# Kernel tuning notes

Hardware: AMD Instinct MI355X
Metric: run time of the kernel (lower is better)

Reference implementation:

```python
import jax, jax.numpy as jnp
import numpy as np

B, N_E, E_DIM = 131072, 1024, 64
BETA = 0.25


def setup_inputs() -> dict:
    key = jax.random.key(0)
    kz, kw = jax.random.split(key)
    z = jax.random.normal(kz, (B, E_DIM), dtype=jnp.float32)
    # nn.Embedding init: uniform(-1/n_e, 1/n_e)
    emb_w = jax.random.uniform(kw, (N_E, E_DIM), dtype=jnp.float32,
                               minval=-1.0 / N_E, maxval=1.0 / N_E)
    return {"z": z, "emb_w": emb_w}


def reference(z, emb_w):
    beta = jnp.float32(BETA)
    # pairwise squared distances: [B, n_e]
    d = (jnp.sum(z * z, axis=1, keepdims=True)
         + jnp.sum(emb_w * emb_w, axis=1)
         - 2.0 * jnp.einsum('bd,nd->bn', z, emb_w))
    idx = jnp.argmin(d, axis=1)                      # [B]
    z_q = jnp.take(emb_w, idx, axis=0)               # [B, e_dim]
    # legacy=False branch
    loss = (beta * jnp.mean((jax.lax.stop_gradient(z_q) - z) ** 2)
            + jnp.mean((z_q - jax.lax.stop_gradient(z)) ** 2))
    # straight-through estimator
    z_q_st = z + jax.lax.stop_gradient(z_q - z)
    # torch.var is unbiased (ddof=1)
    v = jnp.var(idx.astype(jnp.float32), ddof=1)
    return (z_q_st, loss, idx, v)
```

## Files before the change

kernel.cpp:

```cpp
#include <hip/hip_runtime.h>
#include <stdint.h>


typedef __attribute__((ext_vector_type(8))) __bf16 bf16x8;
typedef __attribute__((ext_vector_type(4))) float f32x4;

#define OUT_LOSS 8388608
#define OUT_IDX  8388609
#define OUT_VAR  8519681

#define WS_LOSS  0
#define WS_S1    4096
#define WS_S2    8192
#define WS_EFRAG 12288
#define WS_EE    143360

__device__ __forceinline__ void gld_lds16(const void* g, void* l) {
  __builtin_amdgcn_global_load_lds(
      (const __attribute__((address_space(1))) unsigned*)g,
      (__attribute__((address_space(3))) unsigned*)l, 16, 0, 0);
}

__global__ void vq_prep(const float* __restrict__ emb, char* __restrict__ ws) {
  bf16x8* efrag = (bf16x8*)(ws + WS_EFRAG);
  float* eeoff = (float*)(ws + WS_EE);
  const int t = blockIdx.x;
  const int l = threadIdx.x;
  const int n = t * 16 + (l & 15);
  const int kb0 = (l >> 4) * 8;
  const float* er = emb + n * 64;
  for (int j = 0; j < 2; ++j) {
    const int kb = j * 32 + kb0;
    bf16x8 h;
#pragma unroll
    for (int i = 0; i < 8; ++i) h[i] = (__bf16)(-2.0f * er[kb + i]);
    efrag[(t * 2 + j) * 64 + l] = h;
  }
  if (l < 16) {
    const float* e2 = emb + (t * 16 + l) * 64;
    float s = 0.f;
#pragma unroll
    for (int d = 0; d < 64; ++d) s += e2[d] * e2[d];
    eeoff[t * 16 + l] = s + 0.5f;
  }
}

__global__ void __launch_bounds__(256) vq_main(
    const float* __restrict__ z, const float* __restrict__ emb,
    float* __restrict__ out, char* __restrict__ ws) {
  __shared__ char smfrag[3][16384];
  __shared__ float see[1024];
  __shared__ float sL[4];
  __shared__ int sA[4], sB[4];

  const int tid = threadIdx.x;
  const int wave = tid >> 6, lane = tid & 63;
  const int lr = lane & 15, ksl = lane >> 4;
  const int k0 = ksl * 8;
  const int row_base = blockIdx.x * 256 + wave * 64;

#define STAGE(ph, buf)                                                          \
  {                                                                             \
    _Pragma("unroll")                                                           \
    for (int i_ = 0; i_ < 4; ++i_)                                              \
      gld_lds16(ws + WS_EFRAG + (ph) * 16384 + wave * 4096 + i_ * 1024 + lane * 16, \
                smfrag[buf] + wave * 4096 + i_ * 1024);                         \
  }

  f32x4 zr[16];
#pragma unroll
  for (int r = 0; r < 4; ++r) {
    const float* zp = z + (size_t)(row_base + r * 16 + lr) * 64;
    zr[r * 4 + 0] = *(const f32x4*)(zp + k0);
    zr[r * 4 + 1] = *(const f32x4*)(zp + k0 + 4);
    zr[r * 4 + 2] = *(const f32x4*)(zp + 32 + k0);
    zr[r * 4 + 3] = *(const f32x4*)(zp + 32 + k0 + 4);
  }

  gld_lds16(ws + WS_EE + wave * 1024 + lane * 16, (char*)see + wave * 1024);
  STAGE(0, 0);
  STAGE(1, 1);

  bf16x8 zf[4][2];
  float zz[4];
#pragma unroll
  for (int r = 0; r < 4; ++r) {
    float s = 0.f;
#pragma unroll
    for (int i = 0; i < 4; ++i) {
      zf[r][0][i] = (__bf16)zr[r * 4 + 0][i]; zf[r][0][4 + i] = (__bf16)zr[r * 4 + 1][i];
      zf[r][1][i] = (__bf16)zr[r * 4 + 2][i]; zf[r][1][4 + i] = (__bf16)zr[r * 4 + 3][i];
      s += zr[r * 4 + 0][i] * zr[r * 4 + 0][i] + zr[r * 4 + 1][i] * zr[r * 4 + 1][i]
         + zr[r * 4 + 2][i] * zr[r * 4 + 2][i] + zr[r * 4 + 3][i] * zr[r * 4 + 3][i];
    }
    s += __shfl_xor(s, 16, 64);
    s += __shfl_xor(s, 32, 64);
    zz[r] = s;
  }

  unsigned rk[4];
#pragma unroll
  for (int r = 0; r < 4; ++r) rk[r] = 0xFFFFFFFFu;
  const unsigned kj0 = (unsigned)(ksl * 4), kj1 = kj0 + 1, kj2 = kj0 + 2, kj3 = kj0 + 3;

  for (int ph = 0; ph < 8; ++ph) {
    if (ph < 7) { asm volatile("s_waitcnt vmcnt(4)" ::: "memory"); }
    else        { asm volatile("s_waitcnt vmcnt(0)" ::: "memory"); }
    __builtin_amdgcn_sched_barrier(0);
    __builtin_amdgcn_s_barrier();
    if (ph < 6) STAGE(ph + 2, (ph + 2) % 3);
    const bf16x8* sfrag = (const bf16x8*)(smfrag[ph % 3]);
    __builtin_amdgcn_s_setprio(1);
#pragma unroll
    for (int half = 0; half < 2; ++half) {
      bf16x8 E0[4], E1[4];
      f32x4 EE[4];
#pragma unroll
      for (int q = 0; q < 4; ++q) {
        const int tt = half * 4 + q;
        E0[q] = sfrag[(tt * 2 + 0) * 64 + lane];
        E1[q] = sfrag[(tt * 2 + 1) * 64 + lane];
        EE[q] = *(const f32x4*)(see + (ph * 8 + tt) * 16 + ksl * 4);
      }
#pragma unroll
      for (int q = 0; q < 4; ++q) {
        const unsigned g16 = (unsigned)((ph * 8 + half * 4 + q) * 16);
#pragma unroll
        for (int r = 0; r < 4; ++r) {
          f32x4 a = __builtin_amdgcn_mfma_f32_16x16x32_bf16(E0[q], zf[r][0], EE[q], 0, 0, 0);
          a = __builtin_amdgcn_mfma_f32_16x16x32_bf16(E1[q], zf[r][1], a, 0, 0, 0);
          const unsigned t0 = (__float_as_uint(a[0]) & 0xFFFFFC00u) | kj0;
          const unsigned t1 = (__float_as_uint(a[1]) & 0xFFFFFC00u) | kj1;
          const unsigned t2 = (__float_as_uint(a[2]) & 0xFFFFFC00u) | kj2;
          const unsigned t3 = (__float_as_uint(a[3]) & 0xFFFFFC00u) | kj3;
          const unsigned m = min(min(min(t0, t1), t2), t3);
          rk[r] = min(rk[r], m + g16);
        }
      }
    }
    __builtin_amdgcn_s_setprio(0);
  }
#undef STAGE

#pragma unroll
  for (int r = 0; r < 4; ++r) {
    rk[r] = min(rk[r], (unsigned)__shfl_xor((int)rk[r], 16, 64));
    rk[r] = min(rk[r], (unsigned)__shfl_xor((int)rk[r], 32, 64));
  }

  float ls = 0.f; int s1 = 0, s2 = 0;
  const int erow = lane >> 1, eseg = lane & 1;
  const int src = erow & 15;
  const int hi = erow >> 4;
#pragma unroll
  for (int h = 0; h < 2; ++h) {
    const unsigned ka = (unsigned)__shfl((int)rk[h * 2 + 0], src, 64);
    const unsigned kb = (unsigned)__shfl((int)rk[h * 2 + 1], src, 64);
    const float za = __shfl(zz[h * 2 + 0], src, 64);
    const float zb = __shfl(zz[h * 2 + 1], src, 64);
    const unsigned k = hi ? kb : ka;
    const float zzv = hi ? zb : za;
    const unsigned idx = k & 1023u;
    const size_t rowg = (size_t)row_base + h * 32 + erow;
    const f32x4* ep = (const f32x4*)(emb + (size_t)idx * 64 + eseg * 32);
    f32x4* op = (f32x4*)(out + rowg * 64 + eseg * 32);
#pragma unroll
    for (int c = 0; c < 8; ++c) op[c] = ep[c];
    if (eseg == 0) {
      ls += zzv + __uint_as_float(k & 0xFFFFFC00u) - 0.5f;
      s1 += (int)idx;
      s2 += (int)(idx * idx);
      out[OUT_IDX + rowg] = (float)idx;
    }
  }
#pragma unroll
  for (int off = 1; off < 64; off <<= 1) {
    ls += __shfl_xor(ls, off, 64);
    s1 += __shfl_xor(s1, off, 64);
    s2 += __shfl_xor(s2, off, 64);
  }
  if (lane == 0) { sL[wave] = ls; sA[wave] = s1; sB[wave] = s2; }
  __syncthreads();
  if (tid == 0) {
    float L = 0; int a = 0, b = 0;
#pragma unroll
    for (int w = 0; w < 4; ++w) { L += sL[w]; a += sA[w]; b += sB[w]; }
    ((float*)(ws + WS_LOSS))[blockIdx.x] = L;
    ((int*)(ws + WS_S1))[blockIdx.x] = a;
    ((int*)(ws + WS_S2))[blockIdx.x] = b;
  }
}

__global__ void vq_final(float* __restrict__ out, const char* __restrict__ ws) {
  const int t = threadIdx.x;
  const float* lp = (const float*)(ws + WS_LOSS);
  const int* p1 = (const int*)(ws + WS_S1);
  const int* p2 = (const int*)(ws + WS_S2);
  double L = 0; long long a = 0, b = 0;
#pragma unroll
  for (int kk = 0; kk < 2; ++kk) {
    const int i = t + 256 * kk;
    L += (double)lp[i];
    a += (long long)p1[i];
    b += (long long)p2[i];
  }
#pragma unroll
  for (int off = 1; off < 64; off <<= 1) {
    L += __shfl_xor(L, off, 64);
    a += __shfl_xor(a, off, 64);
    b += __shfl_xor(b, off, 64);
  }
  __shared__ double sLf[4];
  __shared__ long long sAf[4], sBf[4];
  const int wave = t >> 6, lane = t & 63;
  if (lane == 0) { sLf[wave] = L; sAf[wave] = a; sBf[wave] = b; }
  __syncthreads();
  if (t == 0) {
    double Lt = 0; long long at = 0, bt = 0;
#pragma unroll
    for (int w = 0; w < 4; ++w) { Lt += sLf[w]; at += sAf[w]; bt += sBf[w]; }
    out[OUT_LOSS] = (float)(1.25 * Lt / 8388608.0);
    long long num = bt * 131072LL - at * at;
    out[OUT_VAR] = (float)((double)num / (131072.0 * 131071.0));
  }
}

extern "C" void kernel_launch(void* const* d_in, const int* in_sizes, int n_in,
                              void* d_out, int out_size, void* d_ws, size_t ws_size,
                              hipStream_t stream) {
  (void)in_sizes; (void)n_in; (void)out_size; (void)ws_size;
  const float* z = (const float*)d_in[0];
  const float* emb = (const float*)d_in[1];
  float* out = (float*)d_out;
  char* ws = (char*)d_ws;
  vq_prep<<<64, 64, 0, stream>>>(emb, ws);
  vq_main<<<512, 256, 0, stream>>>(z, emb, out, ws);
  vq_final<<<1, 256, 0, stream>>>(out, ws);
}
```

Measured before the change: 48.88 us.

## Split codebook across waves and shrink blocks to 64 rows

```diff
diff --git a/kernel.cpp b/kernel.cpp
--- a/kernel.cpp
+++ b/kernel.cpp
@@ -10,10 +10,10 @@
 #define OUT_VAR  8519681
 
 #define WS_LOSS  0
-#define WS_S1    4096
-#define WS_S2    8192
-#define WS_EFRAG 12288
-#define WS_EE    143360
+#define WS_S1    8192
+#define WS_S2    16384
+#define WS_EFRAG 24576
+#define WS_EE    155648
 
 __device__ __forceinline__ void gld_lds16(const void* g, void* l) {
   __builtin_amdgcn_global_load_lds(
@@ -48,8 +48,10 @@
 __global__ void __launch_bounds__(256) vq_main(
     const float* __restrict__ z, const float* __restrict__ emb,
     float* __restrict__ out, char* __restrict__ ws) {
-  __shared__ char smfrag[3][16384];
+  __shared__ char smfrag[2][4][4096];
   __shared__ float see[1024];
+  __shared__ unsigned skey[4][64];
+  __shared__ float szz[64];
   __shared__ float sL[4];
   __shared__ int sA[4], sB[4];
 
@@ -57,14 +59,15 @@
   const int wave = tid >> 6, lane = tid & 63;
   const int lr = lane & 15, ksl = lane >> 4;
   const int k0 = ksl * 8;
-  const int row_base = blockIdx.x * 256 + wave * 64;
-
-#define STAGE(ph, buf)                                                          \
-  {                                                                             \
-    _Pragma("unroll")                                                           \
-    for (int i_ = 0; i_ < 4; ++i_)                                              \
-      gld_lds16(ws + WS_EFRAG + (ph) * 16384 + wave * 4096 + i_ * 1024 + lane * 16, \
-                smfrag[buf] + wave * 4096 + i_ * 1024);                         \
+  const int row_base = blockIdx.x * 64;
+
+#define STAGE(p, b)                                                            \
+  {                                                                            \
+    _Pragma("unroll")                                                          \
+    for (int i_ = 0; i_ < 4; ++i_)                                             \
+      gld_lds16(ws + WS_EFRAG + (size_t)(wave * 16 + (p) * 2) * 2048           \
+                    + i_ * 1024 + lane * 16,                                   \
+                smfrag[b][wave] + i_ * 1024);                                  \
   }
 
   f32x4 zr[16];
@@ -82,20 +85,26 @@
   STAGE(1, 1);
 
   bf16x8 zf[4][2];
-  float zz[4];
 #pragma unroll
   for (int r = 0; r < 4; ++r) {
-    float s = 0.f;
 #pragma unroll
     for (int i = 0; i < 4; ++i) {
       zf[r][0][i] = (__bf16)zr[r * 4 + 0][i]; zf[r][0][4 + i] = (__bf16)zr[r * 4 + 1][i];
       zf[r][1][i] = (__bf16)zr[r * 4 + 2][i]; zf[r][1][4 + i] = (__bf16)zr[r * 4 + 3][i];
-      s += zr[r * 4 + 0][i] * zr[r * 4 + 0][i] + zr[r * 4 + 1][i] * zr[r * 4 + 1][i]
-         + zr[r * 4 + 2][i] * zr[r * 4 + 2][i] + zr[r * 4 + 3][i] * zr[r * 4 + 3][i];
     }
-    s += __shfl_xor(s, 16, 64);
-    s += __shfl_xor(s, 32, 64);
-    zz[r] = s;
+  }
+  if (wave == 0) {
+#pragma unroll
+    for (int r = 0; r < 4; ++r) {
+      float s = 0.f;
+#pragma unroll
+      for (int i = 0; i < 4; ++i)
+        s += zr[r * 4 + 0][i] * zr[r * 4 + 0][i] + zr[r * 4 + 1][i] * zr[r * 4 + 1][i]
+           + zr[r * 4 + 2][i] * zr[r * 4 + 2][i] + zr[r * 4 + 3][i] * zr[r * 4 + 3][i];
+      s += __shfl_xor(s, 16, 64);
+      s += __shfl_xor(s, 32, 64);
+      if (ksl == 0) szz[r * 16 + lr] = s;
+    }
   }
 
   unsigned rk[4];
@@ -107,38 +116,28 @@
     if (ph < 7) { asm volatile("s_waitcnt vmcnt(4)" ::: "memory"); }
     else        { asm volatile("s_waitcnt vmcnt(0)" ::: "memory"); }
     __builtin_amdgcn_sched_barrier(0);
-    __builtin_amdgcn_s_barrier();
-    if (ph < 6) STAGE(ph + 2, (ph + 2) % 3);
-    const bf16x8* sfrag = (const bf16x8*)(smfrag[ph % 3]);
+    const bf16x8* sf = (const bf16x8*)(smfrag[ph & 1][wave]);
     __builtin_amdgcn_s_setprio(1);
 #pragma unroll
-    for (int half = 0; half < 2; ++half) {
-      bf16x8 E0[4], E1[4];
-      f32x4 EE[4];
-#pragma unroll
-      for (int q = 0; q < 4; ++q) {
-        const int tt = half * 4 + q;
-        E0[q] = sfrag[(tt * 2 + 0) * 64 + lane];
-        E1[q] = sfrag[(tt * 2 + 1) * 64 + lane];
-        EE[q] = *(const f32x4*)(see + (ph * 8 + tt) * 16 + ksl * 4);
-      }
-#pragma unroll
-      for (int q = 0; q < 4; ++q) {
-        const unsigned g16 = (unsigned)((ph * 8 + half * 4 + q) * 16);
-#pragma unroll
-        for (int r = 0; r < 4; ++r) {
-          f32x4 a = __builtin_amdgcn_mfma_f32_16x16x32_bf16(E0[q], zf[r][0], EE[q], 0, 0, 0);
-          a = __builtin_amdgcn_mfma_f32_16x16x32_bf16(E1[q], zf[r][1], a, 0, 0, 0);
-          const unsigned t0 = (__float_as_uint(a[0]) & 0xFFFFFC00u) | kj0;
-          const unsigned t1 = (__float_as_uint(a[1]) & 0xFFFFFC00u) | kj1;
-          const unsigned t2 = (__float_as_uint(a[2]) & 0xFFFFFC00u) | kj2;
-          const unsigned t3 = (__float_as_uint(a[3]) & 0xFFFFFC00u) | kj3;
-          const unsigned m = min(min(min(t0, t1), t2), t3);
-          rk[r] = min(rk[r], m + g16);
-        }
+    for (int t2 = 0; t2 < 2; ++t2) {
+      const int g = wave * 16 + ph * 2 + t2;
+      bf16x8 e0 = sf[(t2 * 2 + 0) * 64 + lane];
+      bf16x8 e1 = sf[(t2 * 2 + 1) * 64 + lane];
+      const f32x4 ee = *(const f32x4*)(see + g * 16 + ksl * 4);
+      const unsigned g16 = (unsigned)(g * 16);
+#pragma unroll
+      for (int r = 0; r < 4; ++r) {
+        f32x4 a = __builtin_amdgcn_mfma_f32_16x16x32_bf16(e0, zf[r][0], ee, 0, 0, 0);
+        a = __builtin_amdgcn_mfma_f32_16x16x32_bf16(e1, zf[r][1], a, 0, 0, 0);
+        const unsigned t0 = (__float_as_uint(a[0]) & 0xFFFFFC00u) | kj0;
+        const unsigned t1 = (__float_as_uint(a[1]) & 0xFFFFFC00u) | kj1;
+        const unsigned t2k = (__float_as_uint(a[2]) & 0xFFFFFC00u) | kj2;
+        const unsigned t3 = (__float_as_uint(a[3]) & 0xFFFFFC00u) | kj3;
+        rk[r] = min(rk[r], min(min(min(t0, t1), t2k), t3) + g16);
       }
     }
     __builtin_amdgcn_s_setprio(0);
+    if (ph < 6) STAGE(ph + 2, ph & 1);
   }
 #undef STAGE
 
@@ -147,31 +146,28 @@
     rk[r] = min(rk[r], (unsigned)__shfl_xor((int)rk[r], 16, 64));
     rk[r] = min(rk[r], (unsigned)__shfl_xor((int)rk[r], 32, 64));
   }
+  if (ksl == 0) {
+#pragma unroll
+    for (int r = 0; r < 4; ++r) skey[wave][r * 16 + lr] = rk[r];
+  }
+  __syncthreads();
+
+  const int row = tid >> 2, seg = tid & 3;
+  const unsigned k = min(min(skey[0][row], skey[1][row]),
+                         min(skey[2][row], skey[3][row]));
+  const unsigned idx = k & 1023u;
+  const size_t rowg = (size_t)row_base + row;
+  const f32x4* ep = (const f32x4*)(emb + (size_t)idx * 64 + seg * 16);
+  f32x4* op = (f32x4*)(out + rowg * 64 + seg * 16);
+#pragma unroll
+  for (int c = 0; c < 4; ++c) op[c] = ep[c];
 
   float ls = 0.f; int s1 = 0, s2 = 0;
-  const int erow = lane >> 1, eseg = lane & 1;
-  const int src = erow & 15;
-  const int hi = erow >> 4;
-#pragma unroll
-  for (int h = 0; h < 2; ++h) {
-    const unsigned ka = (unsigned)__shfl((int)rk[h * 2 + 0], src, 64);
-    const unsigned kb = (unsigned)__shfl((int)rk[h * 2 + 1], src, 64);
-    const float za = __shfl(zz[h * 2 + 0], src, 64);
-    const float zb = __shfl(zz[h * 2 + 1], src, 64);
-    const unsigned k = hi ? kb : ka;
-    const float zzv = hi ? zb : za;
-    const unsigned idx = k & 1023u;
-    const size_t rowg = (size_t)row_base + h * 32 + erow;
-    const f32x4* ep = (const f32x4*)(emb + (size_t)idx * 64 + eseg * 32);
-    f32x4* op = (f32x4*)(out + rowg * 64 + eseg * 32);
-#pragma unroll
-    for (int c = 0; c < 8; ++c) op[c] = ep[c];
-    if (eseg == 0) {
-      ls += zzv + __uint_as_float(k & 0xFFFFFC00u) - 0.5f;
-      s1 += (int)idx;
-      s2 += (int)(idx * idx);
-      out[OUT_IDX + rowg] = (float)idx;
-    }
+  if (seg == 0) {
+    ls = szz[row] + __uint_as_float(k & 0xFFFFFC00u) - 0.5f;
+    s1 = (int)idx;
+    s2 = (int)(idx * idx);
+    out[OUT_IDX + rowg] = (float)idx;
   }
 #pragma unroll
   for (int off = 1; off < 64; off <<= 1) {
@@ -198,7 +194,7 @@
   const int* p2 = (const int*)(ws + WS_S2);
   double L = 0; long long a = 0, b = 0;
 #pragma unroll
-  for (int kk = 0; kk < 2; ++kk) {
+  for (int kk = 0; kk < 8; ++kk) {
     const int i = t + 256 * kk;
     L += (double)lp[i];
     a += (long long)p1[i];
@@ -234,6 +230,6 @@
   float* out = (float*)d_out;
   char* ws = (char*)d_ws;
   vq_prep<<<64, 64, 0, stream>>>(emb, ws);
-  vq_main<<<512, 256, 0, stream>>>(z, emb, out, ws);
+  vq_main<<<2048, 256, 0, stream>>>(z, emb, out, ws);
   vq_final<<<1, 256, 0, stream>>>(out, ws);
 }
```

Result: no change. 49.04 us (+0.3%).
